# Performance work log

Measured on AMD Instinct MI355X. Metric: run time of the kernel, lower is better.

Reference implementation:

```python
import jax, jax.numpy as jnp
import numpy as np

EPS = 0.2          # noise scale (init eps)
N_LAYERS = 3
LAYER_CL = 1
USER_NUM = 100000
ITEM_NUM = 50000
NNZ = 1200000
EMB = 64


def setup_inputs() -> dict:
    key = jax.random.key(0)
    k1, k2, k3, k4, k5, k6 = jax.random.split(key, 6)
    N = USER_NUM + ITEM_NUM
    user_emb = jax.random.normal(k1, (USER_NUM, EMB), dtype=jnp.float32)
    item_emb = jax.random.normal(k2, (ITEM_NUM, EMB), dtype=jnp.float32)
    adj_rows = jax.random.randint(k3, (NNZ,), 0, N, dtype=jnp.int32)
    adj_cols = jax.random.randint(k4, (NNZ,), 0, N, dtype=jnp.int32)
    adj_vals = jax.random.uniform(k5, (NNZ,), dtype=jnp.float32)
    noise = jax.random.uniform(k6, (N_LAYERS, N, EMB), dtype=jnp.float32)  # torch.rand_like per layer
    return {"user_emb": user_emb, "item_emb": item_emb, "adj_rows": adj_rows,
            "adj_cols": adj_cols, "adj_vals": adj_vals, "noise": noise}


def _l2_normalize(x):
    # F.normalize(x, dim=-1): x / max(||x||_2, 1e-12)
    n = jnp.sqrt(jnp.sum(x * x, axis=-1, keepdims=True))
    return x / jnp.maximum(n, 1e-12)


def reference(user_emb, item_emb, adj_rows, adj_cols, adj_vals, noise):
    N = user_emb.shape[0] + item_emb.shape[0]
    ego = jnp.concatenate([user_emb, item_emb], axis=0)  # [N, D]
    acc = jnp.zeros_like(ego)
    cl = ego
    for k in range(N_LAYERS):
        # SpMM: ego <- A @ ego (COO via gather + segment_sum)
        gathered = ego[adj_cols] * adj_vals[:, None]          # [nnz, D]
        ego = jax.ops.segment_sum(gathered, adj_rows, num_segments=N)
        # perturbed=True path: signed, l2-normalized uniform noise
        ego = ego + jnp.sign(ego) * _l2_normalize(noise[k]) * EPS
        acc = acc + ego
        if k == LAYER_CL - 1:
            cl = ego
    final = acc / N_LAYERS  # mean over layers (stack+mean fused)
    u = final[:user_emb.shape[0]]
    i = final[user_emb.shape[0]:]
    u_cl = cl[:user_emb.shape[0]]
    i_cl = cl[user_emb.shape[0]:]
    return (u, i, u_cl, i_cl)
```

## Files before the change

### kernel.cpp

```cpp
#include <hip/hip_runtime.h>

#define EPSV 0.2f
#define USER_NUM 100000
#define ITEM_NUM 50000
#define NTOT 150000
#define NNZ_CNT 1200000
#define EMB 64

#define RPB 128
#define NBUCK ((NTOT + RPB - 1) / RPB)
#define BLKA 512
#define SLICE_E ((NNZ_CNT + BLKA - 1) / BLKA)

#define SCAN_M (NBUCK * BLKA)
#define SCAN_C 4096
#define SCAN_G ((SCAN_M + SCAN_C - 1) / SCAN_C)

typedef float v4f __attribute__((ext_vector_type(4)));
typedef int   v2i __attribute__((ext_vector_type(2)));


__global__ __launch_bounds__(256) void bucket_count_kernel(const int* __restrict__ rows,
                                                           int* __restrict__ bcountT) {
    __shared__ int lh[NBUCK];
    const int t = threadIdx.x, blk = blockIdx.x;
    for (int b = t; b < NBUCK; b += 256) lh[b] = 0;
    __syncthreads();
    const int e0 = blk * SLICE_E;
    const int e1 = (e0 + SLICE_E < NNZ_CNT) ? e0 + SLICE_E : NNZ_CNT;
    for (int e = e0 + t; e < e1; e += 256)
        atomicAdd(&lh[rows[e] >> 7], 1);
    __syncthreads();
    for (int b = t; b < NBUCK; b += 256) bcountT[b * BLKA + blk] = lh[b];
}

__global__ __launch_bounds__(1024) void scan_local_kernel(int* __restrict__ data,
                                                          int* __restrict__ partials) {
    __shared__ int ws[16];
    const int t = threadIdx.x;
    const int base = blockIdx.x * SCAN_C + t * 4;
    int a0 = (base + 0 < SCAN_M) ? data[base + 0] : 0;
    int a1 = (base + 1 < SCAN_M) ? data[base + 1] : 0;
    int a2 = (base + 2 < SCAN_M) ? data[base + 2] : 0;
    int a3 = (base + 3 < SCAN_M) ? data[base + 3] : 0;
    int s = a0 + a1 + a2 + a3;
    int lane = t & 63, wid = t >> 6;
    int inc = s;
    #pragma unroll
    for (int off = 1; off < 64; off <<= 1) {
        int x = __shfl_up(inc, off, 64);
        if (lane >= off) inc += x;
    }
    if (lane == 63) ws[wid] = inc;
    __syncthreads();
    if (t < 16) {
        int w = ws[t];
        #pragma unroll
        for (int off = 1; off < 16; off <<= 1) {
            int x = __shfl_up(w, off, 64);
            if (t >= off) w += x;
        }
        ws[t] = w;
    }
    __syncthreads();
    int texcl = ((wid > 0) ? ws[wid - 1] : 0) + inc - s;
    if (base + 0 < SCAN_M) data[base + 0] = texcl;
    if (base + 1 < SCAN_M) data[base + 1] = texcl + a0;
    if (base + 2 < SCAN_M) data[base + 2] = texcl + a0 + a1;
    if (base + 3 < SCAN_M) data[base + 3] = texcl + a0 + a1 + a2;
    if (t == 1023) partials[blockIdx.x] = texcl + s;
}

__global__ __launch_bounds__(256) void bucket_scatter_kernel(const int* __restrict__ rows,
                                                             const int* __restrict__ cols,
                                                             const float* __restrict__ vals,
                                                             const int* __restrict__ scanT,
                                                             const int* __restrict__ partials,
                                                             int2* __restrict__ ebuf) {
    __shared__ int cur[NBUCK];
    __shared__ int pp[SCAN_G];
    const int t = threadIdx.x, blk = blockIdx.x;
    for (int i = t; i < SCAN_G; i += 256) pp[i] = partials[i];
    __syncthreads();
    if (t == 0) {
        int run = 0;
        for (int i = 0; i < SCAN_G; ++i) { int v = pp[i]; pp[i] = run; run += v; }
    }
    __syncthreads();
    for (int b = t; b < NBUCK; b += 256) {
        int idx = b * BLKA + blk;
        cur[b] = scanT[idx] + pp[idx >> 12];
    }
    __syncthreads();
    const int e0 = blk * SLICE_E;
    const int e1 = (e0 + SLICE_E < NNZ_CNT) ? e0 + SLICE_E : NNZ_CNT;
    for (int e = e0 + t; e < e1; e += 256) {
        int r = rows[e];
        int pos = atomicAdd(&cur[r >> 7], 1);
        ebuf[pos] = make_int2(cols[e] | ((r & 127) << 20), __float_as_int(vals[e]));
    }
}

__global__ __launch_bounds__(256) void bucket_csr_kernel(const int2* __restrict__ ebuf,
                                                         const int* __restrict__ scanT,
                                                         const int* __restrict__ partials,
                                                         int2* __restrict__ rowrange,
                                                         int2* __restrict__ csr) {
    __shared__ int h[RPB];
    __shared__ int c[RPB];
    __shared__ int wst[4];
    __shared__ int pp[SCAN_G];
    const int t = threadIdx.x, b = blockIdx.x;
    for (int i = t; i < SCAN_G; i += 256) pp[i] = partials[i];
    if (t < RPB) h[t] = 0;
    __syncthreads();
    if (t == 0) {
        int run = 0;
        for (int i = 0; i < SCAN_G; ++i) { int v = pp[i]; pp[i] = run; run += v; }
    }
    __syncthreads();
    int i0 = b * BLKA;
    const int base = scanT[i0] + pp[i0 >> 12];
    int next;
    if (b < NBUCK - 1) {
        int i1 = (b + 1) * BLKA;
        next = scanT[i1] + pp[i1 >> 12];
    } else {
        next = NNZ_CNT;
    }
    const int n = next - base;
    for (int i = t; i < n; i += 256)
        atomicAdd(&h[(ebuf[base + i].x >> 20) & 127], 1);
    __syncthreads();
    int lane = t & 63, wid = t >> 6;
    int v = (t < RPB) ? h[t] : 0;
    int inc = v;
    #pragma unroll
    for (int off = 1; off < 64; off <<= 1) {
        int x = __shfl_up(inc, off, 64);
        if (lane >= off) inc += x;
    }
    if (lane == 63) wst[wid] = inc;
    __syncthreads();
    int woff = (wid == 1) ? wst[0] : 0;
    int excl = woff + inc - v;
    if (t < RPB) {
        c[t] = excl;
        int r0 = b * RPB + t;
        if (r0 < NTOT) rowrange[r0] = make_int2(base + excl, base + excl + v);
    }
    __syncthreads();
    for (int i = t; i < n; i += 256) {
        int2 cc = ebuf[base + i];
        int lr = (cc.x >> 20) & 127;
        int pos = atomicAdd(&c[lr], 1);
        csr[base + pos] = make_int2(cc.x & 0xFFFFF, cc.y);
    }
}

template <bool CONCAT, bool FINAL_MODE>
__global__ void spmm_perturb_kernel(const float* __restrict__ src,
                                    const float* __restrict__ user_emb,
                                    const float* __restrict__ item_emb,
                                    const int2* __restrict__ rowrange,
                                    const int2* __restrict__ csr,
                                    const float* __restrict__ noise_k,
                                    const float* __restrict__ e1,
                                    const float* __restrict__ e2,
                                    float* __restrict__ out) {
    int wid = threadIdx.x >> 6;
    int lane = threadIdx.x & 63;
    int rsub = lane >> 4;
    int q = lane & 15;
    int row = blockIdx.x * 16 + wid * 4 + rsub;
    if (row >= NTOT) return;
    int2 rr = rowrange[row];
    int beg = rr.x, end = rr.y;
    size_t rowoff = (size_t)row * EMB;
    v4f nv = __builtin_nontemporal_load((const v4f*)(noise_k + rowoff) + q);
    v4f a1 = (v4f)(0.f);
    v4f a2 = (v4f)(0.f);
    if constexpr (FINAL_MODE) {
        a1 = __builtin_nontemporal_load((const v4f*)(e1 + rowoff) + q);
        a2 = ((const v4f*)(e2 + rowoff))[q];
    }
    const int grp = rsub << 4;
    v4f acc = (v4f)(0.f);
    for (int j = beg; j < end; j += 16) {
        int jj = j + q;
        v2i my = (v2i)(0);
        if (jj < end) my = __builtin_nontemporal_load((const v2i*)csr + jj);
        int c0 = __shfl(my.x, grp, 64);
        for (int half = 0; half < 2; ++half) {
            int u0 = half << 3;
            if (j + u0 >= end) break;
            int nval = end - j - u0; nval = (nval > 8) ? 8 : nval;
            #pragma unroll
            for (int u = 0; u < 8; ++u) {
                int cu = __shfl(my.x, grp + u0 + u, 64);
                float vu = __int_as_float(__shfl(my.y, grp + u0 + u, 64));
                bool ok = (u < nval);
                int c = ok ? cu : c0;
                float vv = ok ? vu : 0.f;
                const float* base;
                if (CONCAT)
                    base = (c < USER_NUM) ? (user_emb + (size_t)c * EMB)
                                          : (item_emb + (size_t)(c - USER_NUM) * EMB);
                else
                    base = src + (size_t)c * EMB;
                v4f x = ((const v4f*)base)[q];
                acc.x = fmaf(vv, x.x, acc.x);
                acc.y = fmaf(vv, x.y, acc.y);
                acc.z = fmaf(vv, x.z, acc.z);
                acc.w = fmaf(vv, x.w, acc.w);
            }
        }
    }
    float s = nv.x * nv.x + nv.y * nv.y + nv.z * nv.z + nv.w * nv.w;
    #pragma unroll
    for (int off = 8; off > 0; off >>= 1) s += __shfl_xor(s, off, 64);
    float scale = EPSV / fmaxf(sqrtf(s), 1e-12f);
    auto pert = [&](float a, float n) {
        float sg = (a > 0.f) ? 1.f : ((a < 0.f) ? -1.f : 0.f);
        return fmaf(sg * scale, n, a);
    };
    v4f y;
    y.x = pert(acc.x, nv.x);
    y.y = pert(acc.y, nv.y);
    y.z = pert(acc.z, nv.z);
    y.w = pert(acc.w, nv.w);
    if constexpr (FINAL_MODE) {
        const float third = 1.f / 3.f;
        v4f f = (a1 + a2 + y) * third;
        __builtin_nontemporal_store(f, (v4f*)(out + rowoff) + q);
    } else {
        ((v4f*)(out + rowoff))[q] = y;
    }
}

extern "C" void kernel_launch(void* const* d_in, const int* in_sizes, int n_in,
                              void* d_out, int out_size, void* d_ws, size_t ws_size,
                              hipStream_t stream) {
    const float* user_emb = (const float*)d_in[0];
    const float* item_emb = (const float*)d_in[1];
    const int*   adj_rows = (const int*)d_in[2];
    const int*   adj_cols = (const int*)d_in[3];
    const float* adj_vals = (const float*)d_in[4];
    const float* noise    = (const float*)d_in[5];

    float* out_final = (float*)d_out;
    float* out_cl    = (float*)d_out + (size_t)NTOT * EMB;

    char* p = (char*)d_ws;
    float* wsA      = (float*)p;  p += (size_t)NTOT * EMB * sizeof(float);
    int2*  rowrange = (int2*)p;   p += (size_t)NTOT * sizeof(int2);
    int2*  csr      = (int2*)p;   p += (size_t)NNZ_CNT * sizeof(int2);

    char* q = (char*)wsA;
    int2* ebuf     = (int2*)q;  q += (size_t)NNZ_CNT * sizeof(int2);
    int*  scanT    = (int*)q;   q += (size_t)SCAN_M * sizeof(int);
    int*  partials = (int*)q;   q += 256 * sizeof(int);

    bucket_count_kernel<<<BLKA, 256, 0, stream>>>(adj_rows, scanT);
    scan_local_kernel<<<SCAN_G, 1024, 0, stream>>>(scanT, partials);
    bucket_scatter_kernel<<<BLKA, 256, 0, stream>>>(adj_rows, adj_cols, adj_vals,
                                                    scanT, partials, ebuf);
    bucket_csr_kernel<<<NBUCK, 256, 0, stream>>>(ebuf, scanT, partials,
                                                 rowrange, csr);

    const int spmm_blocks = (NTOT + 15) / 16;
    const size_t NE = (size_t)NTOT * EMB;

    spmm_perturb_kernel<true, false><<<spmm_blocks, 256, 0, stream>>>(
        nullptr, user_emb, item_emb, rowrange, csr, noise + 0 * NE,
        nullptr, nullptr, out_cl);
    spmm_perturb_kernel<false, false><<<spmm_blocks, 256, 0, stream>>>(
        out_cl, nullptr, nullptr, rowrange, csr, noise + 1 * NE,
        nullptr, nullptr, wsA);
    spmm_perturb_kernel<false, true><<<spmm_blocks, 256, 0, stream>>>(
        wsA, nullptr, nullptr, rowrange, csr, noise + 2 * NE,
        out_cl, wsA, out_final);
}
```

Baseline: 394.9 us.

## Replace per-row CSR build with bucketed SpMM using shared-memory atomic accumulation

Removes the second sort pass that turned row buckets into exact per-row CSR. Bucket granularity drops to 64 rows, and the bucket scatter kernel now records bucket start offsets. The SpMM kernel then processes one bucket per block, gathering source embeddings for each edge and accumulating them into a 64x64 LDS tile with float atomics before applying the perturbation and writing rows out. This saves one preprocessing kernel and its CSR traffic. In exchange, every layer pays many LDS atomic adds instead of accumulating in registers. The scan bounds checks are also dropped because the new sizes divide evenly.

```diff
diff --git a/kernel.cpp b/kernel.cpp
--- a/kernel.cpp
+++ b/kernel.cpp
@@ -7,7 +7,7 @@
 #define NNZ_CNT 1200000
 #define EMB 64
 
-#define RPB 128
+#define RPB 64
 #define NBUCK ((NTOT + RPB - 1) / RPB)
 #define BLKA 512
 #define SLICE_E ((NNZ_CNT + BLKA - 1) / BLKA)
@@ -29,7 +29,7 @@
     const int e0 = blk * SLICE_E;
     const int e1 = (e0 + SLICE_E < NNZ_CNT) ? e0 + SLICE_E : NNZ_CNT;
     for (int e = e0 + t; e < e1; e += 256)
-        atomicAdd(&lh[rows[e] >> 7], 1);
+        atomicAdd(&lh[rows[e] >> 6], 1);
     __syncthreads();
     for (int b = t; b < NBUCK; b += 256) bcountT[b * BLKA + blk] = lh[b];
 }
@@ -39,10 +39,10 @@
     __shared__ int ws[16];
     const int t = threadIdx.x;
     const int base = blockIdx.x * SCAN_C + t * 4;
-    int a0 = (base + 0 < SCAN_M) ? data[base + 0] : 0;
-    int a1 = (base + 1 < SCAN_M) ? data[base + 1] : 0;
-    int a2 = (base + 2 < SCAN_M) ? data[base + 2] : 0;
-    int a3 = (base + 3 < SCAN_M) ? data[base + 3] : 0;
+    int a0 = data[base + 0];
+    int a1 = data[base + 1];
+    int a2 = data[base + 2];
+    int a3 = data[base + 3];
     int s = a0 + a1 + a2 + a3;
     int lane = t & 63, wid = t >> 6;
     int inc = s;
@@ -64,10 +64,10 @@
     }
     __syncthreads();
     int texcl = ((wid > 0) ? ws[wid - 1] : 0) + inc - s;
-    if (base + 0 < SCAN_M) data[base + 0] = texcl;
-    if (base + 1 < SCAN_M) data[base + 1] = texcl + a0;
-    if (base + 2 < SCAN_M) data[base + 2] = texcl + a0 + a1;
-    if (base + 3 < SCAN_M) data[base + 3] = texcl + a0 + a1 + a2;
+    data[base + 0] = texcl;
+    data[base + 1] = texcl + a0;
+    data[base + 2] = texcl + a0 + a1;
+    data[base + 3] = texcl + a0 + a1 + a2;
     if (t == 1023) partials[blockIdx.x] = texcl + s;
 }
 
@@ -76,6 +76,7 @@
                                                              const float* __restrict__ vals,
                                                              const int* __restrict__ scanT,
                                                              const int* __restrict__ partials,
+                                                             int* __restrict__ bucketStart,
                                                              int2* __restrict__ ebuf) {
     __shared__ int cur[NBUCK];
     __shared__ int pp[SCAN_G];
@@ -91,150 +92,110 @@
         int idx = b * BLKA + blk;
         cur[b] = scanT[idx] + pp[idx >> 12];
     }
+    if (blk == 0) {
+        for (int b = t; b < NBUCK; b += 256) {
+            int idx = b * BLKA;
+            bucketStart[b] = scanT[idx] + pp[idx >> 12];
+        }
+        if (t == 0) bucketStart[NBUCK] = NNZ_CNT;
+    }
     __syncthreads();
     const int e0 = blk * SLICE_E;
     const int e1 = (e0 + SLICE_E < NNZ_CNT) ? e0 + SLICE_E : NNZ_CNT;
     for (int e = e0 + t; e < e1; e += 256) {
         int r = rows[e];
-        int pos = atomicAdd(&cur[r >> 7], 1);
-        ebuf[pos] = make_int2(cols[e] | ((r & 127) << 20), __float_as_int(vals[e]));
-    }
-}
-
-__global__ __launch_bounds__(256) void bucket_csr_kernel(const int2* __restrict__ ebuf,
-                                                         const int* __restrict__ scanT,
-                                                         const int* __restrict__ partials,
-                                                         int2* __restrict__ rowrange,
-                                                         int2* __restrict__ csr) {
-    __shared__ int h[RPB];
-    __shared__ int c[RPB];
-    __shared__ int wst[4];
-    __shared__ int pp[SCAN_G];
-    const int t = threadIdx.x, b = blockIdx.x;
-    for (int i = t; i < SCAN_G; i += 256) pp[i] = partials[i];
-    if (t < RPB) h[t] = 0;
-    __syncthreads();
-    if (t == 0) {
-        int run = 0;
-        for (int i = 0; i < SCAN_G; ++i) { int v = pp[i]; pp[i] = run; run += v; }
-    }
-    __syncthreads();
-    int i0 = b * BLKA;
-    const int base = scanT[i0] + pp[i0 >> 12];
-    int next;
-    if (b < NBUCK - 1) {
-        int i1 = (b + 1) * BLKA;
-        next = scanT[i1] + pp[i1 >> 12];
-    } else {
-        next = NNZ_CNT;
-    }
-    const int n = next - base;
-    for (int i = t; i < n; i += 256)
-        atomicAdd(&h[(ebuf[base + i].x >> 20) & 127], 1);
-    __syncthreads();
-    int lane = t & 63, wid = t >> 6;
-    int v = (t < RPB) ? h[t] : 0;
-    int inc = v;
+        int pos = atomicAdd(&cur[r >> 6], 1);
+        ebuf[pos] = make_int2(cols[e] | ((r & 63) << 20), __float_as_int(vals[e]));
+    }
+}
+
+template <bool CONCAT, bool FINAL_MODE>
+__global__ __launch_bounds__(256)
+void spmm_perturb_kernel(const float* __restrict__ src,
+                         const float* __restrict__ user_emb,
+                         const float* __restrict__ item_emb,
+                         const int2* __restrict__ ebuf,
+                         const int* __restrict__ bucketStart,
+                         const float* __restrict__ noise_k,
+                         const float* __restrict__ e1,
+                         const float* __restrict__ e2,
+                         float* __restrict__ out) {
+    __shared__ float acc[RPB * EMB];
+    const int t = threadIdx.x;
+    const int b = blockIdx.x;
+    const int base = bucketStart[b];
+    const int next = bucketStart[b + 1];
+    v4f* acc4 = (v4f*)acc;
     #pragma unroll
-    for (int off = 1; off < 64; off <<= 1) {
-        int x = __shfl_up(inc, off, 64);
-        if (lane >= off) inc += x;
-    }
-    if (lane == 63) wst[wid] = inc;
-    __syncthreads();
-    int woff = (wid == 1) ? wst[0] : 0;
-    int excl = woff + inc - v;
-    if (t < RPB) {
-        c[t] = excl;
-        int r0 = b * RPB + t;
-        if (r0 < NTOT) rowrange[r0] = make_int2(base + excl, base + excl + v);
-    }
-    __syncthreads();
-    for (int i = t; i < n; i += 256) {
-        int2 cc = ebuf[base + i];
-        int lr = (cc.x >> 20) & 127;
-        int pos = atomicAdd(&c[lr], 1);
-        csr[base + pos] = make_int2(cc.x & 0xFFFFF, cc.y);
-    }
-}
-
-template <bool CONCAT, bool FINAL_MODE>
-__global__ void spmm_perturb_kernel(const float* __restrict__ src,
-                                    const float* __restrict__ user_emb,
-                                    const float* __restrict__ item_emb,
-                                    const int2* __restrict__ rowrange,
-                                    const int2* __restrict__ csr,
-                                    const float* __restrict__ noise_k,
-                                    const float* __restrict__ e1,
-                                    const float* __restrict__ e2,
-                                    float* __restrict__ out) {
-    int wid = threadIdx.x >> 6;
-    int lane = threadIdx.x & 63;
-    int rsub = lane >> 4;
-    int q = lane & 15;
-    int row = blockIdx.x * 16 + wid * 4 + rsub;
-    if (row >= NTOT) return;
-    int2 rr = rowrange[row];
-    int beg = rr.x, end = rr.y;
-    size_t rowoff = (size_t)row * EMB;
-    v4f nv = __builtin_nontemporal_load((const v4f*)(noise_k + rowoff) + q);
-    v4f a1 = (v4f)(0.f);
-    v4f a2 = (v4f)(0.f);
-    if constexpr (FINAL_MODE) {
-        a1 = __builtin_nontemporal_load((const v4f*)(e1 + rowoff) + q);
-        a2 = ((const v4f*)(e2 + rowoff))[q];
-    }
-    const int grp = rsub << 4;
-    v4f acc = (v4f)(0.f);
-    for (int j = beg; j < end; j += 16) {
-        int jj = j + q;
-        v2i my = (v2i)(0);
-        if (jj < end) my = __builtin_nontemporal_load((const v2i*)csr + jj);
-        int c0 = __shfl(my.x, grp, 64);
-        for (int half = 0; half < 2; ++half) {
-            int u0 = half << 3;
-            if (j + u0 >= end) break;
-            int nval = end - j - u0; nval = (nval > 8) ? 8 : nval;
+    for (int i = 0; i < (RPB * EMB / 4) / 256; ++i)
+        acc4[t + i * 256] = (v4f)(0.f);
+    __syncthreads();
+    const int g = t >> 4;
+    const int q = t & 15;
+    for (int i = base + g; i < next; i += 32) {
+        int2 ca = ebuf[i];
+        int ib = i + 16;
+        bool hb = ib < next;
+        int2 cb = hb ? ebuf[ib] : ca;
+        int colA = ca.x & 0xFFFFF, lrA = (ca.x >> 20) & (RPB - 1);
+        int colB = cb.x & 0xFFFFF, lrB = (cb.x >> 20) & (RPB - 1);
+        float va = __int_as_float(ca.y);
+        float vb = hb ? __int_as_float(cb.y) : 0.f;
+        const float *sa, *sb;
+        if (CONCAT) {
+            sa = (colA < USER_NUM) ? user_emb + (size_t)colA * EMB
+                                   : item_emb + (size_t)(colA - USER_NUM) * EMB;
+            sb = (colB < USER_NUM) ? user_emb + (size_t)colB * EMB
+                                   : item_emb + (size_t)(colB - USER_NUM) * EMB;
+        } else {
+            sa = src + (size_t)colA * EMB;
+            sb = src + (size_t)colB * EMB;
+        }
+        v4f xa = ((const v4f*)sa)[q];
+        v4f xb = ((const v4f*)sb)[q];
+        float* pa = acc + lrA * EMB + q * 4;
+        float* pb = acc + lrB * EMB + q * 4;
+        atomicAdd(pa + 0, va * xa.x);
+        atomicAdd(pa + 1, va * xa.y);
+        atomicAdd(pa + 2, va * xa.z);
+        atomicAdd(pa + 3, va * xa.w);
+        atomicAdd(pb + 0, vb * xb.x);
+        atomicAdd(pb + 1, vb * xb.y);
+        atomicAdd(pb + 2, vb * xb.z);
+        atomicAdd(pb + 3, vb * xb.w);
+    }
+    __syncthreads();
+    #pragma unroll
+    for (int pass = 0; pass < RPB / 16; ++pass) {
+        int lr = pass * 16 + g;
+        int row = b * RPB + lr;
+        if (row < NTOT) {
+            size_t rowoff = (size_t)row * EMB;
+            v4f a = ((v4f*)(acc + lr * EMB))[q];
+            v4f nv = __builtin_nontemporal_load((const v4f*)(noise_k + rowoff) + q);
+            float s = nv.x * nv.x + nv.y * nv.y + nv.z * nv.z + nv.w * nv.w;
             #pragma unroll
-            for (int u = 0; u < 8; ++u) {
-                int cu = __shfl(my.x, grp + u0 + u, 64);
-                float vu = __int_as_float(__shfl(my.y, grp + u0 + u, 64));
-                bool ok = (u < nval);
-                int c = ok ? cu : c0;
-                float vv = ok ? vu : 0.f;
-                const float* base;
-                if (CONCAT)
-                    base = (c < USER_NUM) ? (user_emb + (size_t)c * EMB)
-                                          : (item_emb + (size_t)(c - USER_NUM) * EMB);
-                else
-                    base = src + (size_t)c * EMB;
-                v4f x = ((const v4f*)base)[q];
-                acc.x = fmaf(vv, x.x, acc.x);
-                acc.y = fmaf(vv, x.y, acc.y);
-                acc.z = fmaf(vv, x.z, acc.z);
-                acc.w = fmaf(vv, x.w, acc.w);
+            for (int off = 8; off > 0; off >>= 1) s += __shfl_xor(s, off, 64);
+            float scale = EPSV / fmaxf(sqrtf(s), 1e-12f);
+            auto pert = [&](float av, float n) {
+                float sg = (av > 0.f) ? 1.f : ((av < 0.f) ? -1.f : 0.f);
+                return fmaf(sg * scale, n, av);
+            };
+            v4f y;
+            y.x = pert(a.x, nv.x);
+            y.y = pert(a.y, nv.y);
+            y.z = pert(a.z, nv.z);
+            y.w = pert(a.w, nv.w);
+            if constexpr (FINAL_MODE) {
+                v4f a1 = __builtin_nontemporal_load((const v4f*)(e1 + rowoff) + q);
+                v4f a2 = ((const v4f*)(e2 + rowoff))[q];
+                const float third = 1.f / 3.f;
+                v4f f = (a1 + a2 + y) * third;
+                __builtin_nontemporal_store(f, (v4f*)(out + rowoff) + q);
+            } else {
+                ((v4f*)(out + rowoff))[q] = y;
             }
         }
-    }
-    float s = nv.x * nv.x + nv.y * nv.y + nv.z * nv.z + nv.w * nv.w;
-    #pragma unroll
-    for (int off = 8; off > 0; off >>= 1) s += __shfl_xor(s, off, 64);
-    float scale = EPSV / fmaxf(sqrtf(s), 1e-12f);
-    auto pert = [&](float a, float n) {
-        float sg = (a > 0.f) ? 1.f : ((a < 0.f) ? -1.f : 0.f);
-        return fmaf(sg * scale, n, a);
-    };
-    v4f y;
-    y.x = pert(acc.x, nv.x);
-    y.y = pert(acc.y, nv.y);
-    y.z = pert(acc.z, nv.z);
-    y.w = pert(acc.w, nv.w);
-    if constexpr (FINAL_MODE) {
-        const float third = 1.f / 3.f;
-        v4f f = (a1 + a2 + y) * third;
-        __builtin_nontemporal_store(f, (v4f*)(out + rowoff) + q);
-    } else {
-        ((v4f*)(out + rowoff))[q] = y;
     }
 }
 
@@ -252,32 +213,27 @@
     float* out_cl    = (float*)d_out + (size_t)NTOT * EMB;
 
     char* p = (char*)d_ws;
-    float* wsA      = (float*)p;  p += (size_t)NTOT * EMB * sizeof(float);
-    int2*  rowrange = (int2*)p;   p += (size_t)NTOT * sizeof(int2);
-    int2*  csr      = (int2*)p;   p += (size_t)NNZ_CNT * sizeof(int2);
-
-    char* q = (char*)wsA;
-    int2* ebuf     = (int2*)q;  q += (size_t)NNZ_CNT * sizeof(int2);
-    int*  scanT    = (int*)q;   q += (size_t)SCAN_M * sizeof(int);
-    int*  partials = (int*)q;   q += 256 * sizeof(int);
+    float* wsA         = (float*)p; p += (size_t)NTOT * EMB * sizeof(float);
+    int2*  ebuf        = (int2*)p;  p += (size_t)NNZ_CNT * sizeof(int2);
+    int*   bucketStart = (int*)p;   p += (size_t)(NBUCK + 1) * sizeof(int);
+
+    int* scanT    = (int*)wsA;
+    int* partials = scanT + SCAN_M;
 
     bucket_count_kernel<<<BLKA, 256, 0, stream>>>(adj_rows, scanT);
     scan_local_kernel<<<SCAN_G, 1024, 0, stream>>>(scanT, partials);
     bucket_scatter_kernel<<<BLKA, 256, 0, stream>>>(adj_rows, adj_cols, adj_vals,
-                                                    scanT, partials, ebuf);
-    bucket_csr_kernel<<<NBUCK, 256, 0, stream>>>(ebuf, scanT, partials,
-                                                 rowrange, csr);
-
-    const int spmm_blocks = (NTOT + 15) / 16;
+                                                    scanT, partials, bucketStart, ebuf);
+
     const size_t NE = (size_t)NTOT * EMB;
 
-    spmm_perturb_kernel<true, false><<<spmm_blocks, 256, 0, stream>>>(
-        nullptr, user_emb, item_emb, rowrange, csr, noise + 0 * NE,
+    spmm_perturb_kernel<true, false><<<NBUCK, 256, 0, stream>>>(
+        nullptr, user_emb, item_emb, ebuf, bucketStart, noise + 0 * NE,
         nullptr, nullptr, out_cl);
-    spmm_perturb_kernel<false, false><<<spmm_blocks, 256, 0, stream>>>(
-        out_cl, nullptr, nullptr, rowrange, csr, noise + 1 * NE,
+    spmm_perturb_kernel<false, false><<<NBUCK, 256, 0, stream>>>(
+        out_cl, nullptr, nullptr, ebuf, bucketStart, noise + 1 * NE,
         nullptr, nullptr, wsA);
-    spmm_perturb_kernel<false, true><<<spmm_blocks, 256, 0, stream>>>(
-        wsA, nullptr, nullptr, rowrange, csr, noise + 2 * NE,
+    spmm_perturb_kernel<false, true><<<NBUCK, 256, 0, stream>>>(
+        wsA, nullptr, nullptr, ebuf, bucketStart, noise + 2 * NE,
         out_cl, wsA, out_final);
 }
```

Result: slower. 1.536 ms (+289.0%).
